# Optimization experiments

Hardware: AMD Instinct MI355X
Metric: run time of the kernel (lower is better)

The kernel has to match this reference:

```python
import jax, jax.numpy as jnp
import numpy as np

B, S, D, H = 2, 2048, 1024, 16
HD = D // H  # head size = 64

def setup_inputs() -> dict:
    key = jax.random.key(0)
    ks = jax.random.split(key, 12)
    sc = 0.02
    return {
        "hidden_states": jax.random.normal(ks[0], (B, S, D), jnp.float32),
        "attention_mask": jnp.zeros((B, S), jnp.float32),  # additive mask (0 = attend)
        "position_bias": jax.random.normal(ks[1], (H, S, S), jnp.float32) * sc,
        "Wq": jax.random.normal(ks[2], (D, D), jnp.float32) * sc,
        "bq": jnp.zeros((D,), jnp.float32),
        "Wk": jax.random.normal(ks[3], (D, D), jnp.float32) * sc,
        "bk": jnp.zeros((D,), jnp.float32),
        "Wv": jax.random.normal(ks[4], (D, D), jnp.float32) * sc,
        "bv": jnp.zeros((D,), jnp.float32),
        "Wo": jax.random.normal(ks[5], (D, D), jnp.float32) * sc,
        "bo": jnp.zeros((D,), jnp.float32),
    }

def reference(hidden_states, attention_mask, position_bias, Wq, bq, Wk, bk, Wv, bv, Wo, bo):
    b, s, _ = hidden_states.shape
    def heads(x):
        # [B,S,D] -> [B,H,S,HD]
        return x.reshape(b, s, H, HD).transpose(0, 2, 1, 3)
    q = heads(hidden_states @ Wq + bq)
    k = heads(hidden_states @ Wk + bk)
    v = heads(hidden_states @ Wv + bv)
    scores = jnp.einsum("bhqd,bhkd->bhqk", q, k) / jnp.sqrt(jnp.float32(HD))
    scores = scores + position_bias[None]                 # [1,H,S,S]
    scores = scores + attention_mask[:, None, None, :]    # [B,1,1,S]
    probs = jax.nn.softmax(scores, axis=-1)
    # dropout is identity in eval mode
    ctx = jnp.einsum("bhqk,bhkd->bhqd", probs, v)
    ctx = ctx.transpose(0, 2, 1, 3).reshape(b, s, D)
    return ctx @ Wo + bo
```

## Files before the change

### kernel.cpp

```cpp
#include <hip/hip_runtime.h>
#include <hip/hip_bf16.h>

#define B_  2
#define S_  2048
#define D_  1024
#define H_  16
#define HD_ 64
#define M_  (B_ * S_)

typedef unsigned short u16;
typedef __attribute__((ext_vector_type(8))) short short8;
typedef __attribute__((ext_vector_type(4))) float f32x4;

#define MFMA16(a, b, c) __builtin_amdgcn_mfma_f32_16x16x32_bf16(a, b, c, 0, 0, 0)

__device__ __forceinline__ u16 f2bf(float f) {
    union { float f; unsigned u; } v; v.f = f;
    unsigned r = v.u + 0x7FFFu + ((v.u >> 16) & 1u);
    return (u16)(r >> 16);
}

__device__ __forceinline__ void gl_lds16(const void* g, void* lds) {
    __builtin_amdgcn_global_load_lds(
        (const __attribute__((address_space(1))) unsigned int*)g,
        (__attribute__((address_space(3))) unsigned int*)lds, 16, 0, 0);
}

__global__ __launch_bounds__(256) void cvt_bf16(const float* __restrict__ x,
                                                u16* __restrict__ y) {
    const int i = (blockIdx.x * 256 + threadIdx.x) * 4;
    const float4 v = *(const float4*)(x + i);
    ushort4 o;
    o.x = f2bf(v.x); o.y = f2bf(v.y); o.z = f2bf(v.z); o.w = f2bf(v.w);
    *(ushort4*)(y + i) = o;
}

__global__ __launch_bounds__(256) void wt_trans(
    const float* __restrict__ w0, const float* __restrict__ w1,
    const float* __restrict__ w2, const float* __restrict__ w3,
    u16* __restrict__ t0, u16* __restrict__ t1,
    u16* __restrict__ t2, u16* __restrict__ t3) {
    const float* W; u16* T;
    switch (blockIdx.z) {
        case 0: W = w0; T = t0; break;
        case 1: W = w1; T = t1; break;
        case 2: W = w2; T = t2; break;
        default: W = w3; T = t3; break;
    }
    __shared__ float t[32][33];
    const int tid = threadIdx.x;
    const int kt = blockIdx.x, nt = blockIdx.y;
    const int r = tid >> 3, c4 = (tid & 7) * 4;
    const float4 v = *(const float4*)&W[(size_t)(kt * 32 + r) * D_ + nt * 32 + c4];
    t[c4 + 0][r] = v.x; t[c4 + 1][r] = v.y; t[c4 + 2][r] = v.z; t[c4 + 3][r] = v.w;
    __syncthreads();
    ushort4 o;
    o.x = f2bf(t[r][c4 + 0]); o.y = f2bf(t[r][c4 + 1]);
    o.z = f2bf(t[r][c4 + 2]); o.w = f2bf(t[r][c4 + 3]);
    *(ushort4*)&T[(size_t)(nt * 32 + r) * D_ + kt * 32 + c4] = o;
}

__global__ __launch_bounds__(256) void v_trans(const u16* __restrict__ V,
                                               u16* __restrict__ VT) {
    __shared__ u16 t[64][72];
    const int bh = blockIdx.x, s0 = blockIdx.y * 64;
    const int tid = threadIdx.x;
    const int ss = tid >> 2, cq = tid & 3;
    const u16* src = V + ((size_t)bh * S_ + s0 + ss) * HD_ + cq * 16;
    u16 buf[16];
    *(uint4*)&buf[0] = *(const uint4*)&src[0];
    *(uint4*)&buf[8] = *(const uint4*)&src[8];
#pragma unroll
    for (int j = 0; j < 16; ++j) t[cq * 16 + j][ss] = buf[j];
    __syncthreads();
    const int dd = tid >> 2;
    u16 ob[16];
#pragma unroll
    for (int j = 0; j < 16; ++j) ob[j] = t[dd][cq * 16 + j];
    u16* dst = VT + ((size_t)bh * HD_ + dd) * S_ + s0 + cq * 16;
    *(uint4*)&dst[0] = *(uint4*)&ob[0];
    *(uint4*)&dst[8] = *(uint4*)&ob[8];
}

__global__ __launch_bounds__(256, 3) void gemm_bt_bf16(
    const u16* __restrict__ A, const u16* __restrict__ Bt,
    const float* __restrict__ bi0, const float* __restrict__ bi1, const float* __restrict__ bi2,
    void* __restrict__ o0, void* __restrict__ o1, void* __restrict__ o2,
    int mode) {
    __shared__ __align__(16) char smem[32768];

    const int tid = threadIdx.x;
    const int wave = tid >> 6, lane = tid & 63;
    const int quad = lane >> 4, l15 = lane & 15;
    const int wm = wave >> 1, wn = wave & 1;
    const int bm = blockIdx.x * 128, bn = blockIdx.y * 128;

    const int sel = bn >> 10;
    const float* bias = (sel == 0) ? bi0 : (sel == 1) ? bi1 : bi2;
    void* outp = (sel == 0) ? o0 : (sel == 1) ? o1 : o2;

    f32x4 acc[4][4];
#pragma unroll
    for (int i = 0; i < 4; ++i)
#pragma unroll
        for (int j = 0; j < 4; ++j) acc[i][j] = (f32x4)0.f;

    const int c0 = wave * 128 + lane;
#pragma unroll
    for (int i = 0; i < 2; ++i) {
        const int c = c0 + i * 64;
        const int row = c >> 2, e = c & 3;
        gl_lds16(A  + (size_t)(bm + row) * D_ + e * 8,
                 smem + (wave * 2 + i) * 1024);
        gl_lds16(Bt + (size_t)(bn + row) * D_ + e * 8,
                 smem + 16384 + (wave * 2 + i) * 1024);
    }
    __syncthreads();

    for (int it = 0; it < 32; ++it) {
        const int cur = it & 1;
        if (it < 31) {
            const int k0n = (it + 1) * 32;
            const int nb = cur ^ 1;
#pragma unroll
            for (int i = 0; i < 2; ++i) {
                const int c = c0 + i * 64;
                const int row = c >> 2, e = c & 3;
                gl_lds16(A  + (size_t)(bm + row) * D_ + k0n + e * 8,
                         smem + nb * 8192 + (wave * 2 + i) * 1024);
                gl_lds16(Bt + (size_t)(bn + row) * D_ + k0n + e * 8,
                         smem + 16384 + nb * 8192 + (wave * 2 + i) * 1024);
            }
        }

        short8 aF[4], bF[4];
#pragma unroll
        for (int mt = 0; mt < 4; ++mt)
            aF[mt] = *(const short8*)(smem + cur * 8192 +
                     ((wm * 64 + mt * 16 + l15) * 32 + quad * 8) * 2);
#pragma unroll
        for (int nt = 0; nt < 4; ++nt)
            bF[nt] = *(const short8*)(smem + 16384 + cur * 8192 +
                     ((wn * 64 + nt * 16 + l15) * 32 + quad * 8) * 2);
#pragma unroll
        for (int mt = 0; mt < 4; ++mt)
#pragma unroll
            for (int nt = 0; nt < 4; ++nt)
                acc[mt][nt] = MFMA16(aF[mt], bF[nt], acc[mt][nt]);

        __syncthreads();
    }

    float bv[4];
#pragma unroll
    for (int nt = 0; nt < 4; ++nt)
        bv[nt] = bias[(bn & 1023) + wn * 64 + nt * 16 + l15];

    if (mode == 1) {
        u16* ob = (u16*)outp;
#pragma unroll
        for (int mt = 0; mt < 4; ++mt)
#pragma unroll
            for (int nt = 0; nt < 4; ++nt)
#pragma unroll
                for (int r = 0; r < 4; ++r) {
                    const int m = bm + wm * 64 + mt * 16 + quad * 4 + r;
                    const int n = (bn & 1023) + wn * 64 + nt * 16 + l15;
                    const int bb = m >> 11, ss = m & (S_ - 1);
                    const int hh = n >> 6,  dd = n & (HD_ - 1);
                    ob[(((size_t)bb * H_ + hh) * S_ + ss) * HD_ + dd] =
                        f2bf(acc[mt][nt][r] + bv[nt]);
                }
    } else {
        float* of = (float*)outp;
#pragma unroll
        for (int mt = 0; mt < 4; ++mt)
#pragma unroll
            for (int nt = 0; nt < 4; ++nt)
#pragma unroll
                for (int r = 0; r < 4; ++r) {
                    const int m = bm + wm * 64 + mt * 16 + quad * 4 + r;
                    const int n = bn + wn * 64 + nt * 16 + l15;
                    of[(size_t)m * D_ + n] = acc[mt][nt][r] + bv[nt];
                }
    }
}

#define PS_OFF   0
#define AK2_OFF  8192
#define AV2_OFF  40960
#define Q1_STAGE 32768

__global__ __launch_bounds__(256, 2) void attn_mfma(
    const u16* __restrict__ Qg, const u16* __restrict__ Kg, const u16* __restrict__ VTg,
    const float* __restrict__ pb, const float* __restrict__ mask,
    u16* __restrict__ Cb) {
    __shared__ __align__(16) char smem[73728];
    u16* PsU = (u16*)(smem + PS_OFF);

    const int tid = threadIdx.x;
    const int wave = tid >> 6, lane = tid & 63;
    const int quad = lane >> 4, l15 = lane & 15;

    const int qblk = blockIdx.x;
    const int h = blockIdx.y;
    const int q0 = qblk * 64;

    const u16* Qb0 = Qg  + (size_t)h        * (S_ * HD_);
    const u16* Qb1 = Qg  + (size_t)(H_ + h) * (S_ * HD_);
    const u16* Kb0 = Kg  + (size_t)h        * (S_ * HD_);
    const u16* Kb1 = Kg  + (size_t)(H_ + h) * (S_ * HD_);
    const u16* VT0 = VTg + (size_t)h        * (HD_ * S_);
    const u16* VT1 = VTg + (size_t)(H_ + h) * (HD_ * S_);

#pragma unroll
    for (int i = 0; i < 2; ++i) {
        const int c = (wave * 2 + i) * 64 + lane;
        const int row = c >> 3, e = c & 7, dc = e ^ (row & 7);
        const int off = (wave * 2 + i) * 1024;
        gl_lds16(Qb0 + (size_t)(q0 + row) * HD_ + dc * 8, smem + PS_OFF + off);
        gl_lds16(Qb1 + (size_t)(q0 + row) * HD_ + dc * 8, smem + Q1_STAGE + off);
        gl_lds16(Kb0 + (size_t)row * HD_ + dc * 8, smem + AK2_OFF + 0 * 8192 + off);
        gl_lds16(Kb1 + (size_t)row * HD_ + dc * 8, smem + AK2_OFF + 1 * 8192 + off);
        gl_lds16(VT0 + (size_t)row * S_ + dc * 8,  smem + AV2_OFF + 0 * 8192 + off);
        gl_lds16(VT1 + (size_t)row * S_ + dc * 8,  smem + AV2_OFF + 1 * 8192 + off);
    }
    __syncthreads();

    short8 aQ[2][2];
#pragma unroll
    for (int kc = 0; kc < 2; ++kc) {
        const int q = wave * 16 + l15;
        const int dc = kc * 4 + quad;
        const int boff = (q * 8 + (dc ^ (q & 7))) * 16;
        aQ[0][kc] = *(const short8*)(smem + PS_OFF + boff);
        aQ[1][kc] = *(const short8*)(smem + Q1_STAGE + boff);
    }

    u16* Pw = PsU + (l15 >> 3) * 512 + (wave * 16 + quad * 4) * 8 + (l15 & 7);

    f32x4 O[2][4];
    float lst[2][4];
#pragma unroll
    for (int bb = 0; bb < 2; ++bb)
#pragma unroll
        for (int nt = 0; nt < 4; ++nt) { O[bb][nt] = (f32x4)0.f; lst[bb][nt] = 0.f; }

    float pbc[4][4], mkc[2][4];
#pragma unroll
    for (int nt = 0; nt < 4; ++nt) {
        mkc[0][nt] = mask[nt * 16 + l15];
        mkc[1][nt] = mask[S_ + nt * 16 + l15];
    }
#pragma unroll
    for (int r = 0; r < 4; ++r) {
        const int qg = q0 + wave * 16 + quad * 4 + r;
        const float* rowp = pb + ((size_t)h * S_ + qg) * S_;
#pragma unroll
        for (int nt = 0; nt < 4; ++nt)
            pbc[r][nt] = __builtin_nontemporal_load(rowp + nt * 16 + l15);
    }

    for (int kt = 0; kt < S_ / 64; ++kt) {
        const int k0 = kt * 64;
        const int cur = kt & 1;
        float pbn[4][4], mkn[2][4];

        if (kt < S_ / 64 - 1) {
            const int nb = cur ^ 1;
            const int k0n = k0 + 64;
#pragma unroll
            for (int i = 0; i < 2; ++i) {
                const int c = (wave * 2 + i) * 64 + lane;
                const int row = c >> 3, e = c & 7, dc = e ^ (row & 7);
                const int off = (wave * 2 + i) * 1024;
                gl_lds16(Kb0 + (size_t)(k0n + row) * HD_ + dc * 8,
                         smem + AK2_OFF + (nb * 2 + 0) * 8192 + off);
                gl_lds16(Kb1 + (size_t)(k0n + row) * HD_ + dc * 8,
                         smem + AK2_OFF + (nb * 2 + 1) * 8192 + off);
                gl_lds16(VT0 + (size_t)row * S_ + k0n + dc * 8,
                         smem + AV2_OFF + (nb * 2 + 0) * 8192 + off);
                gl_lds16(VT1 + (size_t)row * S_ + k0n + dc * 8,
                         smem + AV2_OFF + (nb * 2 + 1) * 8192 + off);
            }
#pragma unroll
            for (int nt = 0; nt < 4; ++nt) {
                mkn[0][nt] = mask[k0n + nt * 16 + l15];
                mkn[1][nt] = mask[S_ + k0n + nt * 16 + l15];
            }
#pragma unroll
            for (int r = 0; r < 4; ++r) {
                const int qg = q0 + wave * 16 + quad * 4 + r;
                const float* rowp = pb + ((size_t)h * S_ + qg) * S_ + k0n;
#pragma unroll
                for (int nt = 0; nt < 4; ++nt)
                    pbn[r][nt] = __builtin_nontemporal_load(rowp + nt * 16 + l15);
            }
        }

#pragma unroll
        for (int bb = 0; bb < 2; ++bb) {
            const int koff = AK2_OFF + (cur * 2 + bb) * 8192;
            const int voff = AV2_OFF + (cur * 2 + bb) * 8192;

            f32x4 sc[4];
#pragma unroll
            for (int nt = 0; nt < 4; ++nt) sc[nt] = (f32x4)0.f;
#pragma unroll
            for (int nt = 0; nt < 4; ++nt)
#pragma unroll
                for (int kc = 0; kc < 2; ++kc) {
                    const int kk = nt * 16 + l15;
                    const int dc = kc * 4 + quad;
                    const short8 bK = *(const short8*)(smem + koff +
                                       (kk * 8 + (dc ^ (kk & 7))) * 16);
                    sc[nt] = MFMA16(aQ[bb][kc], bK, sc[nt]);
                }

#pragma unroll
            for (int r = 0; r < 4; ++r) {
                const float s0 = fmaf(sc[0][r], 0.125f, pbc[r][0] + mkc[bb][0]);
                const float s1 = fmaf(sc[1][r], 0.125f, pbc[r][1] + mkc[bb][1]);
                const float s2 = fmaf(sc[2][r], 0.125f, pbc[r][2] + mkc[bb][2]);
                const float s3 = fmaf(sc[3][r], 0.125f, pbc[r][3] + mkc[bb][3]);
                const float p0 = __expf(s0), p1 = __expf(s1);
                const float p2 = __expf(s2), p3 = __expf(s3);
                lst[bb][r] += (p0 + p1) + (p2 + p3);
                Pw[0 * 1024 + r * 8] = f2bf(p0);
                Pw[1 * 1024 + r * 8] = f2bf(p1);
                Pw[2 * 1024 + r * 8] = f2bf(p2);
                Pw[3 * 1024 + r * 8] = f2bf(p3);
            }

            short8 aP[2];
#pragma unroll
            for (int kc = 0; kc < 2; ++kc)
                aP[kc] = *(const short8*)(PsU + (kc * 4 + quad) * 512 +
                                          (wave * 16 + l15) * 8);
#pragma unroll
            for (int nt = 0; nt < 4; ++nt)
#pragma unroll
                for (int kc = 0; kc < 2; ++kc) {
                    const int d = nt * 16 + l15;
                    const int dc = kc * 4 + quad;
                    const short8 bV = *(const short8*)(smem + voff +
                                       (d * 8 + (dc ^ (d & 7))) * 16);
                    O[bb][nt] = MFMA16(aP[kc], bV, O[bb][nt]);
                }
        }

        if (kt < S_ / 64 - 1) {
#pragma unroll
            for (int r = 0; r < 4; ++r)
#pragma unroll
                for (int nt = 0; nt < 4; ++nt) pbc[r][nt] = pbn[r][nt];
#pragma unroll
            for (int nt = 0; nt < 4; ++nt) {
                mkc[0][nt] = mkn[0][nt]; mkc[1][nt] = mkn[1][nt];
            }
        }
        __syncthreads();
    }

#pragma unroll
    for (int bb = 0; bb < 2; ++bb)
#pragma unroll
        for (int r = 0; r < 4; ++r) {
            float l = lst[bb][r];
#pragma unroll
            for (int off = 1; off < 16; off <<= 1)
                l += __shfl_xor(l, off, 64);
            const float inv = 1.f / l;
            const int s = q0 + wave * 16 + quad * 4 + r;
            u16* dst = Cb + ((size_t)bb * S_ + s) * D_ + h * HD_;
#pragma unroll
            for (int nt = 0; nt < 4; ++nt)
                dst[nt * 16 + l15] = f2bf(O[bb][nt][r] * inv);
        }
}

extern "C" void kernel_launch(void* const* d_in, const int* in_sizes, int n_in,
                              void* d_out, int out_size, void* d_ws, size_t ws_size,
                              hipStream_t stream) {
    const float* X    = (const float*)d_in[0];
    const float* mask = (const float*)d_in[1];
    const float* pb   = (const float*)d_in[2];
    const float* Wq   = (const float*)d_in[3];
    const float* bq   = (const float*)d_in[4];
    const float* Wk   = (const float*)d_in[5];
    const float* bk   = (const float*)d_in[6];
    const float* Wv   = (const float*)d_in[7];
    const float* bv   = (const float*)d_in[8];
    const float* Wo   = (const float*)d_in[9];
    const float* bo   = (const float*)d_in[10];
    float* out = (float*)d_out;

    u16* Xb    = (u16*)d_ws;
    u16* WtQKV = Xb    + (size_t)M_ * D_;
    u16* Wto   = WtQKV + (size_t)3 * D_ * D_;
    u16* Qw    = Wto   + (size_t)D_ * D_;
    u16* Kw    = Qw    + (size_t)M_ * D_;
    u16* Vw    = Kw    + (size_t)M_ * D_;
    u16* Cb    = Vw    + (size_t)M_ * D_;
    u16* VTw   = Cb    + (size_t)M_ * D_;

    cvt_bf16<<<(M_ * D_) / (256 * 4), 256, 0, stream>>>(X, Xb);
    wt_trans<<<dim3(32, 32, 4), 256, 0, stream>>>(
        Wq, Wk, Wv, Wo, WtQKV, WtQKV + (size_t)D_ * D_, WtQKV + (size_t)2 * D_ * D_, Wto);

    gemm_bt_bf16<<<dim3(M_ / 128, 3 * D_ / 128), 256, 0, stream>>>(
        Xb, WtQKV, bq, bk, bv, Qw, Kw, Vw, 1);

    v_trans<<<dim3(B_ * H_, S_ / 64), 256, 0, stream>>>(Vw, VTw);

    attn_mfma<<<dim3(S_ / 64, H_), 256, 0, stream>>>(Qw, Kw, VTw, pb, mask, Cb);

    gemm_bt_bf16<<<dim3(M_ / 128, D_ / 128), 256, 0, stream>>>(
        Cb, Wto, bo, bo, bo, out, out, out, 0);
}
```

Before: 477.4 us.

## Fuse prepass kernels, write V transposed from QKV GEMM epilogue via LDS staging

Merges the X conversion and weight transpose kernels into a single launch. The QKV GEMM epilogue now stages its outputs through LDS so it can write 16-byte coalesced rows. For the V slice it writes the transposed layout directly, which removes the separate v_trans kernel and its extra read and write of V. The costs are a larger shared-memory allocation in the GEMM (36 KB), which may lower occupancy, and an extra LDS round trip in the epilogue.

New measurement: 475.6 us. Within noise of the previous version (-0.4%).

```diff
diff --git a/kernel.cpp b/kernel.cpp
--- a/kernel.cpp
+++ b/kernel.cpp
@@ -26,30 +26,33 @@
         (__attribute__((address_space(3))) unsigned int*)lds, 16, 0, 0);
 }
 
-__global__ __launch_bounds__(256) void cvt_bf16(const float* __restrict__ x,
-                                                u16* __restrict__ y) {
-    const int i = (blockIdx.x * 256 + threadIdx.x) * 4;
-    const float4 v = *(const float4*)(x + i);
-    ushort4 o;
-    o.x = f2bf(v.x); o.y = f2bf(v.y); o.z = f2bf(v.z); o.w = f2bf(v.w);
-    *(ushort4*)(y + i) = o;
-}
-
-__global__ __launch_bounds__(256) void wt_trans(
+__global__ __launch_bounds__(256) void prepass(
+    const float* __restrict__ X, u16* __restrict__ Xb,
     const float* __restrict__ w0, const float* __restrict__ w1,
     const float* __restrict__ w2, const float* __restrict__ w3,
     u16* __restrict__ t0, u16* __restrict__ t1,
     u16* __restrict__ t2, u16* __restrict__ t3) {
+    const int bid = blockIdx.x;
+    const int tid = threadIdx.x;
+    if (bid < 4096) {
+        const int i = (bid * 256 + tid) * 4;
+        const float4 v = *(const float4*)(X + i);
+        ushort4 o;
+        o.x = f2bf(v.x); o.y = f2bf(v.y); o.z = f2bf(v.z); o.w = f2bf(v.w);
+        *(ushort4*)(Xb + i) = o;
+        return;
+    }
+    const int idx = bid - 4096;
+    const int z = idx >> 10, rem = idx & 1023;
+    const int kt = rem >> 5, nt = rem & 31;
     const float* W; u16* T;
-    switch (blockIdx.z) {
+    switch (z) {
         case 0: W = w0; T = t0; break;
         case 1: W = w1; T = t1; break;
         case 2: W = w2; T = t2; break;
         default: W = w3; T = t3; break;
     }
     __shared__ float t[32][33];
-    const int tid = threadIdx.x;
-    const int kt = blockIdx.x, nt = blockIdx.y;
     const int r = tid >> 3, c4 = (tid & 7) * 4;
     const float4 v = *(const float4*)&W[(size_t)(kt * 32 + r) * D_ + nt * 32 + c4];
     t[c4 + 0][r] = v.x; t[c4 + 1][r] = v.y; t[c4 + 2][r] = v.z; t[c4 + 3][r] = v.w;
@@ -60,34 +63,12 @@
     *(ushort4*)&T[(size_t)(nt * 32 + r) * D_ + kt * 32 + c4] = o;
 }
 
-__global__ __launch_bounds__(256) void v_trans(const u16* __restrict__ V,
-                                               u16* __restrict__ VT) {
-    __shared__ u16 t[64][72];
-    const int bh = blockIdx.x, s0 = blockIdx.y * 64;
-    const int tid = threadIdx.x;
-    const int ss = tid >> 2, cq = tid & 3;
-    const u16* src = V + ((size_t)bh * S_ + s0 + ss) * HD_ + cq * 16;
-    u16 buf[16];
-    *(uint4*)&buf[0] = *(const uint4*)&src[0];
-    *(uint4*)&buf[8] = *(const uint4*)&src[8];
-#pragma unroll
-    for (int j = 0; j < 16; ++j) t[cq * 16 + j][ss] = buf[j];
-    __syncthreads();
-    const int dd = tid >> 2;
-    u16 ob[16];
-#pragma unroll
-    for (int j = 0; j < 16; ++j) ob[j] = t[dd][cq * 16 + j];
-    u16* dst = VT + ((size_t)bh * HD_ + dd) * S_ + s0 + cq * 16;
-    *(uint4*)&dst[0] = *(uint4*)&ob[0];
-    *(uint4*)&dst[8] = *(uint4*)&ob[8];
-}
-
 __global__ __launch_bounds__(256, 3) void gemm_bt_bf16(
     const u16* __restrict__ A, const u16* __restrict__ Bt,
     const float* __restrict__ bi0, const float* __restrict__ bi1, const float* __restrict__ bi2,
     void* __restrict__ o0, void* __restrict__ o1, void* __restrict__ o2,
     int mode) {
-    __shared__ __align__(16) char smem[32768];
+    __shared__ __align__(16) char smem[36864];
 
     const int tid = threadIdx.x;
     const int wave = tid >> 6, lane = tid & 63;
@@ -157,20 +138,49 @@
         bv[nt] = bias[(bn & 1023) + wn * 64 + nt * 16 + l15];
 
     if (mode == 1) {
+        u16* tw = (u16*)(smem + wave * 9216);
+        if (sel < 2) {
+#pragma unroll
+            for (int mt = 0; mt < 4; ++mt)
+#pragma unroll
+                for (int nt = 0; nt < 4; ++nt)
+#pragma unroll
+                    for (int r = 0; r < 4; ++r)
+                        tw[(mt * 16 + quad * 4 + r) * 72 + nt * 16 + l15] =
+                            f2bf(acc[mt][nt][r] + bv[nt]);
+        } else {
+#pragma unroll
+            for (int mt = 0; mt < 4; ++mt)
+#pragma unroll
+                for (int nt = 0; nt < 4; ++nt)
+#pragma unroll
+                    for (int r = 0; r < 4; ++r)
+                        tw[(nt * 16 + l15) * 72 + mt * 16 + quad * 4 + r] =
+                            f2bf(acc[mt][nt][r] + bv[nt]);
+        }
         u16* ob = (u16*)outp;
-#pragma unroll
-        for (int mt = 0; mt < 4; ++mt)
-#pragma unroll
-            for (int nt = 0; nt < 4; ++nt)
-#pragma unroll
-                for (int r = 0; r < 4; ++r) {
-                    const int m = bm + wm * 64 + mt * 16 + quad * 4 + r;
-                    const int n = (bn & 1023) + wn * 64 + nt * 16 + l15;
-                    const int bb = m >> 11, ss = m & (S_ - 1);
-                    const int hh = n >> 6,  dd = n & (HD_ - 1);
-                    ob[(((size_t)bb * H_ + hh) * S_ + ss) * HD_ + dd] =
-                        f2bf(acc[mt][nt][r] + bv[nt]);
-                }
+        const int hh = ((bn & 1023) + wn * 64) >> 6;
+        const int rrow = lane >> 3, cc = (lane & 7) * 8;
+        if (sel < 2) {
+#pragma unroll
+            for (int i = 0; i < 8; ++i) {
+                const int row = i * 8 + rrow;
+                const uint4 val = *(const uint4*)(tw + row * 72 + cc);
+                const int m = bm + wm * 64 + row;
+                const int bb = m >> 11, ss = m & (S_ - 1);
+                *(uint4*)&ob[(((size_t)bb * H_ + hh) * S_ + ss) * HD_ + cc] = val;
+            }
+        } else {
+            const int mbase = bm + wm * 64;
+            const int bb = mbase >> 11;
+            const int ss = (mbase & (S_ - 1)) + cc;
+#pragma unroll
+            for (int i = 0; i < 8; ++i) {
+                const int row = i * 8 + rrow;
+                const uint4 val = *(const uint4*)(tw + row * 72 + cc);
+                *(uint4*)&ob[(((size_t)bb * H_ + hh) * HD_ + row) * S_ + ss] = val;
+            }
+        }
     } else {
         float* of = (float*)outp;
 #pragma unroll
@@ -400,18 +410,15 @@
     u16* Wto   = WtQKV + (size_t)3 * D_ * D_;
     u16* Qw    = Wto   + (size_t)D_ * D_;
     u16* Kw    = Qw    + (size_t)M_ * D_;
-    u16* Vw    = Kw    + (size_t)M_ * D_;
-    u16* Cb    = Vw    + (size_t)M_ * D_;
-    u16* VTw   = Cb    + (size_t)M_ * D_;
-
-    cvt_bf16<<<(M_ * D_) / (256 * 4), 256, 0, stream>>>(X, Xb);
-    wt_trans<<<dim3(32, 32, 4), 256, 0, stream>>>(
-        Wq, Wk, Wv, Wo, WtQKV, WtQKV + (size_t)D_ * D_, WtQKV + (size_t)2 * D_ * D_, Wto);
+    u16* VTw   = Kw    + (size_t)M_ * D_;
+    u16* Cb    = VTw   + (size_t)M_ * D_;
+
+    prepass<<<8192, 256, 0, stream>>>(
+        X, Xb, Wq, Wk, Wv, Wo,
+        WtQKV, WtQKV + (size_t)D_ * D_, WtQKV + (size_t)2 * D_ * D_, Wto);
 
     gemm_bt_bf16<<<dim3(M_ / 128, 3 * D_ / 128), 256, 0, stream>>>(
-        Xb, WtQKV, bq, bk, bv, Qw, Kw, Vw, 1);
-
-    v_trans<<<dim3(B_ * H_, S_ / 64), 256, 0, stream>>>(Vw, VTw);
+        Xb, WtQKV, bq, bk, bv, Qw, Kw, VTw, 1);
 
     attn_mfma<<<dim3(S_ / 64, H_), 256, 0, stream>>>(Qw, Kw, VTw, pb, mask, Cb);
 
```
